# Kernel optimization log

Hardware: AMD Instinct MI355X
Metric: run time of the kernel (lower is better)

## Reference

```python
import jax, jax.numpy as jnp
import numpy as np

V = 512      # visible_size (channel_size, reverse_nodes=False)
H = 512      # hidden_size
FULL = V + H # full_size = 1024
T = 128      # timesteps
LAM = 0.5    # params['lambda']


def _build_lambda():
    # Lambda: (V, FULL); first V cols = lambda, hidden cols = 1, diagonal = 1
    Lam = jnp.concatenate([jnp.full((V, V), LAM, jnp.float32),
                           jnp.ones((V, H), jnp.float32)], axis=1)
    idx = jnp.arange(V)
    return Lam.at[idx, idx].set(1.0)


def setup_inputs() -> dict:
    key = jax.random.key(0)
    k1, k2, k3 = jax.random.split(key, 3)
    X = jax.random.normal(k1, (T, V), jnp.float32)
    W = jax.random.normal(k2, (FULL, FULL), jnp.float32) / np.float32(np.sqrt(FULL))
    b = jax.random.normal(k3, (FULL,), jnp.float32) * 0.01
    return {"X": X, "W": W, "b": b}


def reference(X, W, b):
    Lam = _build_lambda()          # (V, FULL)
    one_minus = 1.0 - Lam[:, :V]   # (V, V); zero on diagonal

    def step(carry, x_t):
        R, _ = carry
        WR = R @ W.T + b                           # Linear: (V, FULL)
        U = Lam * WR                               # masked recurrent part
        # Y has x_t broadcast across rows in first V cols, zeros elsewhere
        U = U.at[:, :V].add(one_minus * x_t[None, :])
        return (jax.nn.relu(U), U), None           # R = phi(U)

    init = (jnp.zeros((V, FULL), jnp.float32), jnp.zeros((V, FULL), jnp.float32))
    (_, U_last), _ = jax.lax.scan(step, init, X)
    return jnp.diagonal(U_last[:, :V])             # (V,)
```

## Files before the change

kernel.cpp:

```cpp
#include <hip/hip_runtime.h>
#include <stdint.h>

#define Vv 512
#define Ff 1024

typedef unsigned short u16;
typedef unsigned long long u64;
typedef __attribute__((ext_vector_type(8))) short s16x8;
typedef __attribute__((ext_vector_type(4))) float f32x4;

#define OFF_WH  (0ull)
#define OFF_WM  (2ull << 20)
#define OFF_WL  (4ull << 20)
#define OFF_A0  (6ull << 20)
#define OFF_A1  (9ull << 20)
#define OFF_FLG (12ull << 20)


__device__ __forceinline__ void split3(float v, u16& h, u16& m, u16& l) {
    unsigned u = __float_as_uint(v);
    float fh = __uint_as_float(u & 0xFFFF0000u);
    h = (u16)(u >> 16);
    float r1 = v - fh;
    unsigned u1 = __float_as_uint(r1);
    float fm = __uint_as_float(u1 & 0xFFFF0000u);
    m = (u16)(u1 >> 16);
    float r2 = r1 - fm;
    l = (u16)(__float_as_uint(r2) >> 16);
}

__device__ __forceinline__ float bf2f(short v) {
    return __uint_as_float(((unsigned)(u16)v) << 16);
}

__global__ void wsplit_kernel(const float* __restrict__ W, char* __restrict__ ws) {
    int idx = blockIdx.x * 256 + threadIdx.x;
    int j = idx >> 7, ko = idx & 127;
    const float* wr = W + (size_t)j * Ff + ko * 8;
    s16x8 vh, vm, vl;
#pragma unroll
    for (int e = 0; e < 8; ++e) {
        u16 h, m, l; split3(wr[e], h, m, l);
        vh[e] = (short)h; vm[e] = (short)m; vl[e] = (short)l;
    }
    int js = j >> 6, nq = (j >> 4) & 3, col = j & 15;
    int c = ko >> 3, kh = (ko >> 2) & 1, o = ko & 3;
    unsigned uhm = (unsigned)((((js * 4 + nq) * 16 + c) * 2 + kh) * 64 + o * 16 + col);
    unsigned ul  = (unsigned)(js * 8192 + (c * 2 + kh) * 256 + o * 64 + nq * 16 + col);
    *(s16x8*)(ws + OFF_WH + (size_t)uhm * 16) = vh;
    *(s16x8*)(ws + OFF_WM + (size_t)uhm * 16) = vm;
    *(s16x8*)(ws + OFF_WL + (size_t)ul * 16)  = vl;
}

__global__ void init_kernel(const float* __restrict__ X, const float* __restrict__ b,
                            char* __restrict__ ws) {
    int idx = blockIdx.x * 256 + threadIdx.x;
    if (idx < 4096) ((unsigned*)(ws + OFF_FLG))[idx] = 0u;
    int i = idx >> 7, jo = idx & 127;
    s16x8 vh, vm, vl;
#pragma unroll
    for (int e = 0; e < 8; ++e) {
        int j = jo * 8 + e;
        float u = b[j];
        if (j < Vv && i != j) u = 0.5f * u + 0.5f * X[j];
        u = fmaxf(u, 0.f);
        u16 h, m, l; split3(u, h, m, l);
        vh[e] = (short)h; vm[e] = (short)m; vl[e] = (short)l;
    }
    int ig = i >> 5, r = i & 31, js = jo >> 3, o = jo & 7;
    size_t tb = (size_t)(ig * 16 + js) * 12288 + (size_t)(o * 32 + r) * 16;
    *(s16x8*)(ws + OFF_A0 + tb)        = vh;
    *(s16x8*)(ws + OFF_A0 + tb + 4096) = vm;
    *(s16x8*)(ws + OFF_A0 + tb + 8192) = vl;
}

#define GST(addr, val) \
    asm volatile("global_store_dwordx2 %0, %1, off sc0 sc1" \
                 :: "v"((void*)(addr)), "v"(val) : "memory")
#define MM(acc_, a_, b_) \
    asm("v_mfma_f32_16x16x32_bf16 %0, %1, %2, %0" : "+v"(acc_) : "v"(a_), "v"(b_))

__global__ __launch_bounds__(512, 2)
void mega_kernel(const float* __restrict__ X, const float* __restrict__ b,
                 char* __restrict__ ws) {
    extern __shared__ char smem[];
    const int tid = threadIdx.x, bid = blockIdx.x;
    const int ig = bid >> 4, js = bid & 15;
    const int lane = tid & 63, l15 = lane & 15, l4 = lane >> 4;
    const int w = tid >> 6, kh = w & 1, nq = w >> 1;

    unsigned* flg = (unsigned*)(ws + OFF_FLG);

    {
        const char* src = ws + OFF_WL + (size_t)js * 131072;
#pragma unroll
        for (int q = 0; q < 16; ++q) {
            unsigned u = (unsigned)(q * 512 + tid) * 16u;
            __builtin_amdgcn_global_load_lds(
                (const __attribute__((address_space(1))) void*)(src + u),
                (__attribute__((address_space(3))) void*)(smem + u), 16, 0, 0);
        }
    }

    s16x8 Bh0, Bh1, Bh2, Bh3, Bh4, Bh5, Bh6, Bh7, Bh8, Bh9, Bh10, Bh11, Bh12, Bh13, Bh14, Bh15;
    s16x8 Bm0, Bm1, Bm2, Bm3, Bm4, Bm5, Bm6, Bm7, Bm8, Bm9, Bm10, Bm11, Bm12, Bm13, Bm14, Bm15;
    {
        const char* wfrag = ws + OFF_WH +
            (size_t)(((((js * 4 + nq) * 16) * 2 + kh) * 64) + l4 * 16 + l15) * 16;
#define LOADW(n) do {                                                                  \
        const char* wp_ = wfrag + (size_t)(((js + (n)) & 15) * 2048);                  \
        asm volatile("global_load_dwordx4 %0, %1, off"                                 \
                     : "=v"(Bh##n) : "v"((const void*)wp_));                           \
        asm volatile("global_load_dwordx4 %0, %1, off"                                 \
                     : "=v"(Bm##n) : "v"((const void*)(wp_ + (2ull << 20))));          \
    } while (0)
        LOADW(0);  LOADW(1);  LOADW(2);  LOADW(3);
        LOADW(4);  LOADW(5);  LOADW(6);  LOADW(7);
        LOADW(8);  LOADW(9);  LOADW(10); LOADW(11);
        LOADW(12); LOADW(13); LOADW(14); LOADW(15);
#undef LOADW
    }

    const int row = (tid >> 1) & 31;
    const int c4 = ((tid >> 6) << 3) + ((tid & 1) << 2);
    const int i_glob = ig * 32 + row;
    const float4 bbv = *(const float4*)(b + js * 64 + c4);
    float* red = (float*)(smem + 131072);
    const unsigned ownoff = (unsigned)tid * 8u;

    const unsigned abase = (unsigned)(((kh * 4 + l4) * 32 + l15) * 16);
    const unsigned a00 = abase,          a01 = abase + 256;
    const unsigned a10 = abase + 4096,   a11 = abase + 4096 + 256;
    const unsigned a20 = abase + 8192,   a21 = abase + 8192 + 256;
    const unsigned bloff = (unsigned)(kh * 4096 + (l4 * 64 + nq * 16 + l15) * 16);

    s16x8 Af00, Af01, Af10, Af11, Af20, Af21, Bl;
    u64 ga0, ga1, ga2, gb0, gb1, gb2, gc0, gc1, gc2;

#define GLDA3(g0_, g1_, g2_, cc) do {                                                  \
        const char* ap_ = tb + (size_t)((cc) * 12288) + (size_t)tid * 8;               \
        asm volatile("global_load_dwordx2 %0, %1, off sc0 sc1"                         \
                     : "=v"(g0_) : "v"((const void*)ap_) : "memory");                  \
        asm volatile("global_load_dwordx2 %0, %1, off sc0 sc1"                         \
                     : "=v"(g1_) : "v"((const void*)(ap_ + 4096)) : "memory");         \
        asm volatile("global_load_dwordx2 %0, %1, off sc0 sc1"                         \
                     : "=v"(g2_) : "v"((const void*)(ap_ + 8192)) : "memory");         \
    } while (0)
#define DSWR3(slot, g0_, g1_, g2_) do {                                                \
        char* wp_ = smem + 131072 + (slot) * 12288 + (size_t)tid * 8;                  \
        *(u64*)(wp_) = g0_; *(u64*)(wp_ + 4096) = g1_; *(u64*)(wp_ + 8192) = g2_;      \
    } while (0)
#define DSRD7(slot, cc) do {                                                           \
        const char* sb_ = smem + 131072 + (slot) * 12288;                              \
        Af00 = *(const s16x8*)(sb_ + a00); Af01 = *(const s16x8*)(sb_ + a01);          \
        Af10 = *(const s16x8*)(sb_ + a10); Af11 = *(const s16x8*)(sb_ + a11);          \
        Af20 = *(const s16x8*)(sb_ + a20); Af21 = *(const s16x8*)(sb_ + a21);          \
        Bl = *(const s16x8*)(smem + (size_t)((cc) * 8192) + bloff);                    \
    } while (0)
#define MFMA12(n) do {                                                                 \
        __builtin_amdgcn_s_setprio(1);                                                 \
        MM(acc0, Af00, Bh##n); MM(acc1, Af01, Bh##n);                                  \
        MM(acc0, Af00, Bm##n); MM(acc1, Af01, Bm##n);                                  \
        MM(acc0, Af10, Bh##n); MM(acc1, Af11, Bh##n);                                  \
        MM(acc0, Af00, Bl);    MM(acc1, Af01, Bl);                                     \
        MM(acc0, Af20, Bh##n); MM(acc1, Af21, Bh##n);                                  \
        MM(acc0, Af10, Bm##n); MM(acc1, Af11, Bm##n);                                  \
        __builtin_amdgcn_s_setprio(0);                                                 \
    } while (0)
#define CHUNK(n, P0, P1, P2, Q0, Q1, Q2, VM) do {                                      \
        __builtin_amdgcn_sched_barrier(0);                                             \
        MFMA12(n);                                                                     \
        __builtin_amdgcn_sched_barrier(0);                                             \
        asm volatile("s_waitcnt vmcnt(" #VM ")" ::: "memory");                         \
        DSWR3(((n) + 1) & 1, Q0, Q1, Q2);                                              \
        asm volatile("s_waitcnt lgkmcnt(0)" ::: "memory");                             \
        __builtin_amdgcn_s_barrier();                                                  \
        DSRD7(((n) + 1) & 1, (js + (n) + 1) & 15);                                     \
    } while (0)

    {
        const char* own0 = ws + OFF_A0 + (size_t)(ig * 16 + js) * 12288;
        const char* tb = own0;
        GLDA3(ga0, ga1, ga2, 0);
        asm volatile("s_waitcnt vmcnt(0)" ::: "memory");
        DSWR3(0, ga0, ga1, ga2);
    }
    __syncthreads();

    for (int t = 1; t <= 126; ++t) {
        char* srcA = ws + ((t & 1) ? OFF_A0 : OFF_A1);
        char* dstA = ws + ((t & 1) ? OFF_A1 : OFF_A0);
        const char* tb = srcA + (size_t)ig * 16 * 12288;

        DSRD7(0, js);

        if (lane < 16) {
            while ((int)__hip_atomic_load(&flg[(ig * 16 + lane) * 16], __ATOMIC_RELAXED,
                                          __HIP_MEMORY_SCOPE_AGENT) < t - 1)
                __builtin_amdgcn_s_sleep(1);
        }
        asm volatile("" ::: "memory");

        GLDA3(gb0, gb1, gb2, (js + 1) & 15);
        GLDA3(gc0, gc1, gc2, (js + 2) & 15);

        f32x4 acc0 = (f32x4){0.f, 0.f, 0.f, 0.f};
        f32x4 acc1 = (f32x4){0.f, 0.f, 0.f, 0.f};

        GLDA3(ga0, ga1, ga2, (js + 3) & 15);
        CHUNK(0,  ga0, ga1, ga2, gb0, gb1, gb2, 6);
        GLDA3(gb0, gb1, gb2, (js + 4) & 15);
        CHUNK(1,  gb0, gb1, gb2, gc0, gc1, gc2, 6);
        GLDA3(gc0, gc1, gc2, (js + 5) & 15);
        CHUNK(2,  gc0, gc1, gc2, ga0, ga1, ga2, 6);
        GLDA3(ga0, ga1, ga2, (js + 6) & 15);
        CHUNK(3,  ga0, ga1, ga2, gb0, gb1, gb2, 6);
        GLDA3(gb0, gb1, gb2, (js + 7) & 15);
        CHUNK(4,  gb0, gb1, gb2, gc0, gc1, gc2, 6);
        GLDA3(gc0, gc1, gc2, (js + 8) & 15);
        CHUNK(5,  gc0, gc1, gc2, ga0, ga1, ga2, 6);
        GLDA3(ga0, ga1, ga2, (js + 9) & 15);
        CHUNK(6,  ga0, ga1, ga2, gb0, gb1, gb2, 6);
        GLDA3(gb0, gb1, gb2, (js + 10) & 15);
        CHUNK(7,  gb0, gb1, gb2, gc0, gc1, gc2, 6);
        GLDA3(gc0, gc1, gc2, (js + 11) & 15);
        CHUNK(8,  gc0, gc1, gc2, ga0, ga1, ga2, 6);
        GLDA3(ga0, ga1, ga2, (js + 12) & 15);
        CHUNK(9,  ga0, ga1, ga2, gb0, gb1, gb2, 6);
        GLDA3(gb0, gb1, gb2, (js + 13) & 15);
        CHUNK(10, gb0, gb1, gb2, gc0, gc1, gc2, 6);
        GLDA3(gc0, gc1, gc2, (js + 14) & 15);
        CHUNK(11, gc0, gc1, gc2, ga0, ga1, ga2, 6);
        GLDA3(ga0, ga1, ga2, (js + 15) & 15);
        CHUNK(12, ga0, ga1, ga2, gb0, gb1, gb2, 6);
        CHUNK(13, ga0, ga1, ga2, gc0, gc1, gc2, 3);
        CHUNK(14, ga0, ga1, ga2, ga0, ga1, ga2, 0);
        MFMA12(15);

        __builtin_amdgcn_s_barrier();
        asm volatile("s_nop 7\n\ts_nop 7");

#pragma unroll
        for (int r = 0; r < 4; ++r)
            red[kh * 2176 + (l4 * 4 + r) * 68 + nq * 16 + l15] = acc0[r];
#pragma unroll
        for (int r = 0; r < 4; ++r)
            red[kh * 2176 + (16 + l4 * 4 + r) * 68 + nq * 16 + l15] = acc1[r];
        __syncthreads();

        float4 p0 = *(const float4*)&red[row * 68 + c4];
        float4 p1 = *(const float4*)&red[2176 + row * 68 + c4];
        __syncthreads();

        {
            float s0 = p0.x + p1.x, s1 = p0.y + p1.y, s2 = p0.z + p1.z, s3 = p0.w + p1.w;
            const float* xt = X + (size_t)t * Vv;
            float u0 = s0 + bbv.x, u1 = s1 + bbv.y, u2 = s2 + bbv.z, u3 = s3 + bbv.w;
            if (js < 8) {
                int j0 = js * 64 + c4;
                float x0 = xt[j0], x1 = xt[j0 + 1], x2 = xt[j0 + 2], x3 = xt[j0 + 3];
                if (i_glob != j0)     u0 = 0.5f * u0 + 0.5f * x0;
                if (i_glob != j0 + 1) u1 = 0.5f * u1 + 0.5f * x1;
                if (i_glob != j0 + 2) u2 = 0.5f * u2 + 0.5f * x2;
                if (i_glob != j0 + 3) u3 = 0.5f * u3 + 0.5f * x3;
            }
            u0 = fmaxf(u0, 0.f); u1 = fmaxf(u1, 0.f);
            u2 = fmaxf(u2, 0.f); u3 = fmaxf(u3, 0.f);
            u16 h0, m0, l0, h1, m1, l1, h2, m2, l2, h3, m3, l3;
            split3(u0, h0, m0, l0); split3(u1, h1, m1, l1);
            split3(u2, h2, m2, l2); split3(u3, h3, m3, l3);
            u64 ph = (u64)h0 | ((u64)h1 << 16) | ((u64)h2 << 32) | ((u64)h3 << 48);
            u64 pm = (u64)m0 | ((u64)m1 << 16) | ((u64)m2 << 32) | ((u64)m3 << 48);
            u64 pl = (u64)l0 | ((u64)l1 << 16) | ((u64)l2 << 32) | ((u64)l3 << 48);
            size_t tbo = (size_t)(ig * 16 + js) * 12288 + ownoff;
            GST(dstA + tbo, ph);
            GST(dstA + tbo + 4096, pm);
            GST(dstA + tbo + 8192, pl);
            *(u64*)(smem + 131072 + ownoff) = ph;
            *(u64*)(smem + 131072 + ownoff + 4096) = pm;
            *(u64*)(smem + 131072 + ownoff + 8192) = pl;
        }
        asm volatile("s_waitcnt vmcnt(0)" ::: "memory");
        __syncthreads();
        if (tid == 0)
            __hip_atomic_store(&flg[(ig * 16 + js) * 16], (unsigned)t, __ATOMIC_RELAXED,
                               __HIP_MEMORY_SCOPE_AGENT);
    }
#undef GLDA3
#undef DSWR3
#undef DSRD7
#undef MFMA12
#undef CHUNK
}

__global__ void diag_kernel(const char* __restrict__ ws, const float* __restrict__ W,
                            const float* __restrict__ b, float* __restrict__ out) {
    int i = blockIdx.x, lane = threadIdx.x;
    const char* A0 = ws + OFF_A0;
    float s = 0.f;
#pragma unroll
    for (int rep = 0; rep < 2; ++rep) {
        int ko = lane + rep * 64;
        int js = ko >> 3, o = ko & 7;
        size_t tb = (size_t)((i >> 5) * 16 + js) * 12288
                  + (size_t)(o * 32 + (i & 31)) * 16;
        s16x8 vh = *(const s16x8*)(A0 + tb);
        s16x8 vm = *(const s16x8*)(A0 + tb + 4096);
        s16x8 vl = *(const s16x8*)(A0 + tb + 8192);
        const float* wr = W + (size_t)i * Ff + ko * 8;
#pragma unroll
        for (int e = 0; e < 8; ++e)
            s += (bf2f(vh[e]) + bf2f(vm[e]) + bf2f(vl[e])) * wr[e];
    }
#pragma unroll
    for (int off = 32; off > 0; off >>= 1) s += __shfl_down(s, off);
    if (lane == 0) out[i] = s + b[i];
}

extern "C" void kernel_launch(void* const* d_in, const int* in_sizes, int n_in,
                              void* d_out, int out_size, void* d_ws, size_t ws_size,
                              hipStream_t stream) {
    const float* X = (const float*)d_in[0];
    const float* W = (const float*)d_in[1];
    const float* b = (const float*)d_in[2];
    float* out = (float*)d_out;
    char* ws = (char*)d_ws;

    hipFuncSetAttribute(reinterpret_cast<const void*>(mega_kernel),
                        hipFuncAttributeMaxDynamicSharedMemorySize, 155648);

    wsplit_kernel<<<512, 256, 0, stream>>>(W, ws);
    init_kernel<<<256, 256, 0, stream>>>(X, b, ws);
    mega_kernel<<<256, 512, 155648, stream>>>(X, b, ws);
    diag_kernel<<<512, 64, 0, stream>>>(ws, W, b, out);
}
```

Measured before the change: 904.7 us.

## Stream W hi/mid fragments per chunk instead of holding all in registers

Previously each thread held all 16 hi and 16 mid W fragments in registers for the whole kernel. Now the fragments are reloaded from global memory every timestep through a three-deep rotating register buffer, interleaved with the activation prefetch pipeline. This frees a large number of VGPRs, which may ease register pressure or spilling. In exchange it adds repeated global or L2 traffic for W on every step and makes the vmcnt accounting in the pipeline more intricate.

```diff
diff --git a/kernel.cpp b/kernel.cpp
--- a/kernel.cpp
+++ b/kernel.cpp
@@ -102,24 +102,8 @@
         }
     }
 
-    s16x8 Bh0, Bh1, Bh2, Bh3, Bh4, Bh5, Bh6, Bh7, Bh8, Bh9, Bh10, Bh11, Bh12, Bh13, Bh14, Bh15;
-    s16x8 Bm0, Bm1, Bm2, Bm3, Bm4, Bm5, Bm6, Bm7, Bm8, Bm9, Bm10, Bm11, Bm12, Bm13, Bm14, Bm15;
-    {
-        const char* wfrag = ws + OFF_WH +
-            (size_t)(((((js * 4 + nq) * 16) * 2 + kh) * 64) + l4 * 16 + l15) * 16;
-#define LOADW(n) do {                                                                  \
-        const char* wp_ = wfrag + (size_t)(((js + (n)) & 15) * 2048);                  \
-        asm volatile("global_load_dwordx4 %0, %1, off"                                 \
-                     : "=v"(Bh##n) : "v"((const void*)wp_));                           \
-        asm volatile("global_load_dwordx4 %0, %1, off"                                 \
-                     : "=v"(Bm##n) : "v"((const void*)(wp_ + (2ull << 20))));          \
-    } while (0)
-        LOADW(0);  LOADW(1);  LOADW(2);  LOADW(3);
-        LOADW(4);  LOADW(5);  LOADW(6);  LOADW(7);
-        LOADW(8);  LOADW(9);  LOADW(10); LOADW(11);
-        LOADW(12); LOADW(13); LOADW(14); LOADW(15);
-#undef LOADW
-    }
+    const char* wfrag = ws + OFF_WH +
+        (size_t)(((((js * 4 + nq) * 16) * 2 + kh) * 64) + l4 * 16 + l15) * 16;
 
     const int row = (tid >> 1) & 31;
     const int c4 = ((tid >> 6) << 3) + ((tid & 1) << 2);
@@ -135,8 +119,20 @@
     const unsigned bloff = (unsigned)(kh * 4096 + (l4 * 64 + nq * 16 + l15) * 16);
 
     s16x8 Af00, Af01, Af10, Af11, Af20, Af21, Bl;
+    s16x8 Wha, Wma, Whb, Wmb, Whc, Wmc;
     u64 ga0, ga1, ga2, gb0, gb1, gb2, gc0, gc1, gc2;
 
+#define SB __builtin_amdgcn_sched_barrier(0)
+#define VMC(N) asm volatile("s_waitcnt vmcnt(" #N ")" ::: "memory")
+#define LGKM asm volatile("s_waitcnt lgkmcnt(0)" ::: "memory")
+#define BAR __builtin_amdgcn_s_barrier()
+#define GLDW(H_, M_, nn) do {                                                          \
+        const char* wp_ = wfrag + (size_t)((((js + (nn)) & 15)) * 2048);               \
+        asm volatile("global_load_dwordx4 %0, %1, off"                                 \
+                     : "=v"(H_) : "v"((const void*)wp_) : "memory");                   \
+        asm volatile("global_load_dwordx4 %0, %1, off"                                 \
+                     : "=v"(M_) : "v"((const void*)(wp_ + (2ull << 20))) : "memory");  \
+    } while (0)
 #define GLDA3(g0_, g1_, g2_, cc) do {                                                  \
         const char* ap_ = tb + (size_t)((cc) * 12288) + (size_t)tid * 8;               \
         asm volatile("global_load_dwordx2 %0, %1, off sc0 sc1"                         \
@@ -157,32 +153,30 @@
         Af20 = *(const s16x8*)(sb_ + a20); Af21 = *(const s16x8*)(sb_ + a21);          \
         Bl = *(const s16x8*)(smem + (size_t)((cc) * 8192) + bloff);                    \
     } while (0)
-#define MFMA12(n) do {                                                                 \
+#define MFMA12W(H_, M_) do {                                                           \
         __builtin_amdgcn_s_setprio(1);                                                 \
-        MM(acc0, Af00, Bh##n); MM(acc1, Af01, Bh##n);                                  \
-        MM(acc0, Af00, Bm##n); MM(acc1, Af01, Bm##n);                                  \
-        MM(acc0, Af10, Bh##n); MM(acc1, Af11, Bh##n);                                  \
-        MM(acc0, Af00, Bl);    MM(acc1, Af01, Bl);                                     \
-        MM(acc0, Af20, Bh##n); MM(acc1, Af21, Bh##n);                                  \
-        MM(acc0, Af10, Bm##n); MM(acc1, Af11, Bm##n);                                  \
+        MM(acc0, Af00, H_); MM(acc1, Af01, H_);                                        \
+        MM(acc0, Af00, M_); MM(acc1, Af01, M_);                                        \
+        MM(acc0, Af10, H_); MM(acc1, Af11, H_);                                        \
+        MM(acc0, Af00, Bl); MM(acc1, Af01, Bl);                                        \
+        MM(acc0, Af20, H_); MM(acc1, Af21, H_);                                        \
+        MM(acc0, Af10, M_); MM(acc1, Af11, M_);                                        \
         __builtin_amdgcn_s_setprio(0);                                                 \
     } while (0)
-#define CHUNK(n, P0, P1, P2, Q0, Q1, Q2, VM) do {                                      \
-        __builtin_amdgcn_sched_barrier(0);                                             \
-        MFMA12(n);                                                                     \
-        __builtin_amdgcn_sched_barrier(0);                                             \
-        asm volatile("s_waitcnt vmcnt(" #VM ")" ::: "memory");                         \
-        DSWR3(((n) + 1) & 1, Q0, Q1, Q2);                                              \
-        asm volatile("s_waitcnt lgkmcnt(0)" ::: "memory");                             \
-        __builtin_amdgcn_s_barrier();                                                  \
+#define CHUNKW(n, PA0, PA1, PA2, H_, M_, QA0, QA1, QA2, VM) do {                       \
+        GLDA3(PA0, PA1, PA2, (js + (n) + 3) & 15);                                     \
+        SB; MFMA12W(H_, M_); SB;                                                       \
+        GLDW(H_, M_, (n) + 3);                                                         \
+        VMC(VM);                                                                       \
+        DSWR3(((n) + 1) & 1, QA0, QA1, QA2);                                           \
+        LGKM; BAR;                                                                     \
         DSRD7(((n) + 1) & 1, (js + (n) + 1) & 15);                                     \
     } while (0)
 
     {
-        const char* own0 = ws + OFF_A0 + (size_t)(ig * 16 + js) * 12288;
-        const char* tb = own0;
+        const char* tb = ws + OFF_A0 + (size_t)(ig * 16 + js) * 12288;
         GLDA3(ga0, ga1, ga2, 0);
-        asm volatile("s_waitcnt vmcnt(0)" ::: "memory");
+        VMC(0);
         DSWR3(0, ga0, ga1, ga2);
     }
     __syncthreads();
@@ -191,6 +185,10 @@
         char* srcA = ws + ((t & 1) ? OFF_A0 : OFF_A1);
         char* dstA = ws + ((t & 1) ? OFF_A1 : OFF_A0);
         const char* tb = srcA + (size_t)ig * 16 * 12288;
+
+        GLDW(Wha, Wma, 0);
+        GLDW(Whb, Wmb, 1);
+        GLDW(Whc, Wmc, 2);
 
         DSRD7(0, js);
 
@@ -208,36 +206,49 @@
         f32x4 acc1 = (f32x4){0.f, 0.f, 0.f, 0.f};
 
         GLDA3(ga0, ga1, ga2, (js + 3) & 15);
-        CHUNK(0,  ga0, ga1, ga2, gb0, gb1, gb2, 6);
+        VMC(9);
+        SB; MFMA12W(Wha, Wma); SB;
+        GLDW(Wha, Wma, 3);
+        VMC(8);
+        DSWR3(1, gb0, gb1, gb2);
+        LGKM; BAR;
+        DSRD7(1, (js + 1) & 15);
+
         GLDA3(gb0, gb1, gb2, (js + 4) & 15);
-        CHUNK(1,  gb0, gb1, gb2, gc0, gc1, gc2, 6);
-        GLDA3(gc0, gc1, gc2, (js + 5) & 15);
-        CHUNK(2,  gc0, gc1, gc2, ga0, ga1, ga2, 6);
-        GLDA3(ga0, ga1, ga2, (js + 6) & 15);
-        CHUNK(3,  ga0, ga1, ga2, gb0, gb1, gb2, 6);
-        GLDA3(gb0, gb1, gb2, (js + 7) & 15);
-        CHUNK(4,  gb0, gb1, gb2, gc0, gc1, gc2, 6);
-        GLDA3(gc0, gc1, gc2, (js + 8) & 15);
-        CHUNK(5,  gc0, gc1, gc2, ga0, ga1, ga2, 6);
-        GLDA3(ga0, ga1, ga2, (js + 9) & 15);
-        CHUNK(6,  ga0, ga1, ga2, gb0, gb1, gb2, 6);
-        GLDA3(gb0, gb1, gb2, (js + 10) & 15);
-        CHUNK(7,  gb0, gb1, gb2, gc0, gc1, gc2, 6);
-        GLDA3(gc0, gc1, gc2, (js + 11) & 15);
-        CHUNK(8,  gc0, gc1, gc2, ga0, ga1, ga2, 6);
-        GLDA3(ga0, ga1, ga2, (js + 12) & 15);
-        CHUNK(9,  ga0, ga1, ga2, gb0, gb1, gb2, 6);
-        GLDA3(gb0, gb1, gb2, (js + 13) & 15);
-        CHUNK(10, gb0, gb1, gb2, gc0, gc1, gc2, 6);
-        GLDA3(gc0, gc1, gc2, (js + 14) & 15);
-        CHUNK(11, gc0, gc1, gc2, ga0, ga1, ga2, 6);
-        GLDA3(ga0, ga1, ga2, (js + 15) & 15);
-        CHUNK(12, ga0, ga1, ga2, gb0, gb1, gb2, 6);
-        CHUNK(13, ga0, ga1, ga2, gc0, gc1, gc2, 3);
-        CHUNK(14, ga0, ga1, ga2, ga0, ga1, ga2, 0);
-        MFMA12(15);
-
-        __builtin_amdgcn_s_barrier();
+        SB; MFMA12W(Whb, Wmb); SB;
+        GLDW(Whb, Wmb, 4);
+        VMC(10);
+        DSWR3(0, gc0, gc1, gc2);
+        LGKM; BAR;
+        DSRD7(0, (js + 2) & 15);
+
+        CHUNKW(2,  gc0, gc1, gc2, Whc, Wmc, ga0, ga1, ga2, 10);
+        CHUNKW(3,  ga0, ga1, ga2, Wha, Wma, gb0, gb1, gb2, 10);
+        CHUNKW(4,  gb0, gb1, gb2, Whb, Wmb, gc0, gc1, gc2, 10);
+        CHUNKW(5,  gc0, gc1, gc2, Whc, Wmc, ga0, ga1, ga2, 10);
+        CHUNKW(6,  ga0, ga1, ga2, Wha, Wma, gb0, gb1, gb2, 10);
+        CHUNKW(7,  gb0, gb1, gb2, Whb, Wmb, gc0, gc1, gc2, 10);
+        CHUNKW(8,  gc0, gc1, gc2, Whc, Wmc, ga0, ga1, ga2, 10);
+        CHUNKW(9,  ga0, ga1, ga2, Wha, Wma, gb0, gb1, gb2, 10);
+        CHUNKW(10, gb0, gb1, gb2, Whb, Wmb, gc0, gc1, gc2, 10);
+        CHUNKW(11, gc0, gc1, gc2, Whc, Wmc, ga0, ga1, ga2, 10);
+        CHUNKW(12, ga0, ga1, ga2, Wha, Wma, gb0, gb1, gb2, 10);
+
+        SB; MFMA12W(Whb, Wmb); SB;
+        VMC(5);
+        DSWR3(0, gc0, gc1, gc2);
+        LGKM; BAR;
+        DSRD7(0, (js + 14) & 15);
+
+        SB; MFMA12W(Whc, Wmc); SB;
+        VMC(0);
+        DSWR3(1, ga0, ga1, ga2);
+        LGKM; BAR;
+        DSRD7(1, (js + 15) & 15);
+
+        SB; MFMA12W(Wha, Wma); SB;
+
+        BAR;
         asm volatile("s_nop 7\n\ts_nop 7");
 
 #pragma unroll
@@ -280,17 +291,22 @@
             *(u64*)(smem + 131072 + ownoff + 4096) = pm;
             *(u64*)(smem + 131072 + ownoff + 8192) = pl;
         }
-        asm volatile("s_waitcnt vmcnt(0)" ::: "memory");
+        VMC(0);
         __syncthreads();
         if (tid == 0)
             __hip_atomic_store(&flg[(ig * 16 + js) * 16], (unsigned)t, __ATOMIC_RELAXED,
                                __HIP_MEMORY_SCOPE_AGENT);
     }
+#undef SB
+#undef VMC
+#undef LGKM
+#undef BAR
+#undef GLDW
 #undef GLDA3
 #undef DSWR3
 #undef DSRD7
-#undef MFMA12
-#undef CHUNK
+#undef MFMA12W
+#undef CHUNKW
 }
 
 __global__ void diag_kernel(const char* __restrict__ ws, const float* __restrict__ W,
```

Result: slower. 1.123 ms (+24.1%).
